# Kernel tuning notes

Measured on AMD Instinct MI355X. Metric: run time of the kernel, lower is better.

Reference implementation:

```python
import jax, jax.numpy as jnp
import numpy as np

MARGIN = 0.3

def _cdist(x):
    # pairwise euclidean distances, safe sqrt (zero grad at 0)
    sq = jnp.sum(x * x, axis=1)
    d2 = sq[:, None] + sq[None, :] - 2.0 * (x @ x.T)
    d2 = jnp.maximum(d2, 0.0)
    safe = jnp.where(d2 > 0, d2, 1.0)
    return jnp.where(d2 > 0, jnp.sqrt(safe), 0.0)

def setup_inputs() -> dict:
    key = jax.random.key(0)
    k1, k2 = jax.random.split(key)
    embeddings = jax.random.normal(k1, (4096, 128), dtype=jnp.float32)
    labels = jax.random.randint(k2, (4096,), 0, 256)
    return {"embeddings": embeddings, "labels": labels}

def reference(embeddings, labels):
    B = embeddings.shape[0]
    dist = _cdist(embeddings)                      # [B, B]
    same = labels[:, None] == labels[None, :]      # [B, B]
    eye = jnp.eye(B, dtype=bool)
    pos_mask = same & ~eye
    neg_mask = ~same
    neg_inf = jnp.array(-jnp.inf, dist.dtype)
    pos_inf = jnp.array(jnp.inf, dist.dtype)
    hard_pos = jnp.max(jnp.where(pos_mask, dist, neg_inf), axis=1)  # [B]
    hard_neg = jnp.min(jnp.where(neg_mask, dist, pos_inf), axis=1)  # [B]
    valid = jnp.any(pos_mask, axis=1) & jnp.any(neg_mask, axis=1)
    per_row = jax.nn.relu(hard_pos - hard_neg + MARGIN)
    per_row = jnp.where(valid, per_row, 0.0)
    num_valid = jnp.sum(valid.astype(dist.dtype))
    return jnp.sum(per_row) / jnp.maximum(num_valid, 1.0)
```

## Files before the change

kernel.cpp:

```cpp
#include <hip/hip_runtime.h>
#include <hip/hip_bf16.h>


typedef __attribute__((ext_vector_type(8))) short short8;
typedef __attribute__((ext_vector_type(4))) float f32x4;

#define MARGIN_F 0.3f
#define NEG_BIG -3.4e38f
#define POS_BIG 3.4e38f
#define WAITVM(N) __builtin_amdgcn_s_waitcnt(((N)&15)|((((N)>>4)&3)<<14)|(7<<4)|(15<<8))

__device__ __forceinline__ void gl_lds16(const void* g, void* l) {
    __builtin_amdgcn_global_load_lds(
        (const __attribute__((address_space(1))) void*)g,
        (__attribute__((address_space(3))) void*)l, 16, 0, 0);
}

__device__ inline unsigned short f2bf(float x) {
    union { __hip_bfloat16 h; unsigned short u; } c;
    c.h = __float2bfloat16(x);
    return c.u;
}

__global__ __launch_bounds__(256) void tl_prep(const float* __restrict__ E,
                                               unsigned short* __restrict__ Ebf,
                                               float* __restrict__ sqn,
                                               unsigned* __restrict__ cnt) {
    int t = blockIdx.x * 256 + threadIdx.x;
    if (t < 4) cnt[t] = 0u;
    int row = t >> 5;
    int kq = (t & 31) * 4;
    float4 v = *(const float4*)&E[(size_t)row * 128 + kq];
    float s = fmaf(v.x, v.x, fmaf(v.y, v.y, fmaf(v.z, v.z, v.w * v.w)));
    ushort4 h4;
    h4.x = f2bf(v.x); h4.y = f2bf(v.y); h4.z = f2bf(v.z); h4.w = f2bf(v.w);
    *(ushort4*)&Ebf[(size_t)row * 128 + kq] = h4;
#pragma unroll
    for (int m = 1; m < 32; m <<= 1) s += __shfl_xor(s, m);
    if ((t & 31) == 0) sqn[row] = s;
}

__global__ __launch_bounds__(256, 4) void tl_phase1(const unsigned short* __restrict__ Ebf,
                                                    const int* __restrict__ labels,
                                                    const float* __restrict__ sqn,
                                                    float* __restrict__ pmp,
                                                    float* __restrict__ pmn) {
    union SM {
        struct { unsigned short A[128 * 64]; unsigned short B[128 * 64]; } s;
        struct { float mp[128][32]; float mn[128][32]; } f;
    };
    __shared__ __align__(16) SM sm;

    const int tid = threadIdx.x;
    const int l = tid & 63, w = tid >> 6;
    const int wr = w >> 1, wc = w & 1;
    const int q = l >> 4, r16 = l & 15;
    const int i0 = blockIdx.x * 128, j0 = blockIdx.y * 128;

    const unsigned short* gA[4];
    const unsigned short* gB[4];
#pragma unroll
    for (int t2 = 0; t2 < 4; ++t2) {
        int s = w * 256 + t2 * 64 + l;
        int row = s >> 3, ch = (s & 7) ^ (row & 7);
        gA[t2] = Ebf + (size_t)(i0 + row) * 128 + ch * 8;
        gB[t2] = Ebf + (size_t)(j0 + row) * 128 + ch * 8;
    }

    int li[4][4], lj[4];
    float sj[4];
#pragma unroll
    for (int ti = 0; ti < 4; ++ti)
#pragma unroll
        for (int p = 0; p < 4; ++p)
            li[ti][p] = labels[i0 + wr * 64 + ti * 16 + q * 4 + p];
#pragma unroll
    for (int tj = 0; tj < 4; ++tj) {
        int cj = j0 + wc * 64 + tj * 16 + r16;
        lj[tj] = labels[cj];
        sj[tj] = sqn[cj];
    }

    f32x4 acc[4][4];
#pragma unroll
    for (int ti = 0; ti < 4; ++ti)
#pragma unroll
        for (int tj = 0; tj < 4; ++tj) acc[ti][tj] = (f32x4)0.0f;

#pragma unroll
    for (int kc = 0; kc < 2; ++kc) {
        __syncthreads();
#pragma unroll
        for (int t2 = 0; t2 < 4; ++t2) {
            gl_lds16(gA[t2] + kc * 64, &sm.s.A[w * 2048 + t2 * 512]);
            gl_lds16(gB[t2] + kc * 64, &sm.s.B[w * 2048 + t2 * 512]);
        }
        WAITVM(0);
        __builtin_amdgcn_s_barrier();
#pragma unroll
        for (int s = 0; s < 2; ++s) {
            short8 af[4], bf[4];
            const int cA = ((s * 4 + q) ^ (r16 & 7)) * 8;
#pragma unroll
            for (int t2 = 0; t2 < 4; ++t2) {
                af[t2] = *(const short8*)&sm.s.A[(wr * 64 + t2 * 16 + r16) * 64 + cA];
                bf[t2] = *(const short8*)&sm.s.B[(wc * 64 + t2 * 16 + r16) * 64 + cA];
            }
#pragma unroll
            for (int ti = 0; ti < 4; ++ti)
#pragma unroll
                for (int tj = 0; tj < 4; ++tj)
                    acc[ti][tj] = __builtin_amdgcn_mfma_f32_16x16x32_bf16(
                        af[ti], bf[tj], acc[ti][tj], 0, 0, 0);
        }
    }

    float mp[4][4], mn[4][4];
#pragma unroll
    for (int ti = 0; ti < 4; ++ti)
#pragma unroll
        for (int p = 0; p < 4; ++p) { mp[ti][p] = NEG_BIG; mn[ti][p] = POS_BIG; }
    const bool diagblk = (blockIdx.x == blockIdx.y);
#pragma unroll
    for (int tj = 0; tj < 4; ++tj) {
#pragma unroll
        for (int ti = 0; ti < 4; ++ti)
#pragma unroll
            for (int p = 0; p < 4; ++p) {
                float val = fmaf(-2.0f, acc[ti][tj][p], sj[tj]);
                bool same = (li[ti][p] == lj[tj]);
                bool self = diagblk &&
                    ((wr * 64 + ti * 16 + q * 4 + p) == (wc * 64 + tj * 16 + r16));
                mp[ti][p] = fmaxf(mp[ti][p], (same && !self) ? val : NEG_BIG);
                mn[ti][p] = fminf(mn[ti][p], same ? POS_BIG : val);
            }
    }

    __syncthreads();
#pragma unroll
    for (int ti = 0; ti < 4; ++ti)
#pragma unroll
        for (int p = 0; p < 4; ++p) {
            int rloc = wr * 64 + ti * 16 + q * 4 + p;
            sm.f.mp[rloc][wc * 16 + r16] = mp[ti][p];
            sm.f.mn[rloc][wc * 16 + r16] = mn[ti][p];
        }
    __syncthreads();
    {
        int row = tid >> 1, hf = tid & 1;
        const float4* P = (const float4*)&sm.f.mp[row][hf * 16];
        const float4* N = (const float4*)&sm.f.mn[row][hf * 16];
        float4 p0 = P[0], p1 = P[1], p2 = P[2], p3 = P[3];
        float4 n0 = N[0], n1 = N[1], n2 = N[2], n3 = N[3];
        float M = fmaxf(fmaxf(fmaxf(p0.x, p0.y), fmaxf(p0.z, p0.w)),
                        fmaxf(fmaxf(p1.x, p1.y), fmaxf(p1.z, p1.w)));
        M = fmaxf(M, fmaxf(fmaxf(fmaxf(p2.x, p2.y), fmaxf(p2.z, p2.w)),
                           fmaxf(fmaxf(p3.x, p3.y), fmaxf(p3.z, p3.w))));
        float m_ = fminf(fminf(fminf(n0.x, n0.y), fminf(n0.z, n0.w)),
                         fminf(fminf(n1.x, n1.y), fminf(n1.z, n1.w)));
        m_ = fminf(m_, fminf(fminf(fminf(n2.x, n2.y), fminf(n2.z, n2.w)),
                             fminf(fminf(n3.x, n3.y), fminf(n3.z, n3.w))));
        M = fmaxf(M, __shfl_xor(M, 1));
        m_ = fminf(m_, __shfl_xor(m_, 1));
        if (hf == 0) {
            pmp[(size_t)blockIdx.y * 4096 + i0 + row] = M;
            pmn[(size_t)blockIdx.y * 4096 + i0 + row] = m_;
        }
    }
}

__global__ __launch_bounds__(256) void tl_phase2(const float* __restrict__ pmp,
                                                 const float* __restrict__ pmn,
                                                 const float* __restrict__ sqn,
                                                 unsigned* __restrict__ cnt,
                                                 float* __restrict__ accum,
                                                 float* __restrict__ out) {
    __shared__ float sp[4], sv[4];
    int tid = threadIdx.x;
    int r = blockIdx.x * 256 + tid;
    float mp = NEG_BIG, mn = POS_BIG;
#pragma unroll
    for (int k = 0; k < 32; ++k) {
        mp = fmaxf(mp, pmp[(size_t)k * 4096 + r]);
        mn = fminf(mn, pmn[(size_t)k * 4096 + r]);
    }
    float si = sqn[r];
    bool valid = (mp > 0.5f * NEG_BIG) && (mn < 0.5f * POS_BIG);
    float hp = sqrtf(fmaxf(si + mp, 0.0f));
    float hn = sqrtf(fmaxf(si + mn, 0.0f));
    float pr = fmaxf(hp - hn + MARGIN_F, 0.0f);
    float s = valid ? pr : 0.0f;
    float n = valid ? 1.0f : 0.0f;
#pragma unroll
    for (int m = 1; m < 64; m <<= 1) {
        s += __shfl_xor(s, m);
        n += __shfl_xor(n, m);
    }
    if ((tid & 63) == 0) { sp[tid >> 6] = s; sv[tid >> 6] = n; }
    __syncthreads();
    if (tid == 0) {
        atomicAdd(&accum[0], sp[0] + sp[1] + sp[2] + sp[3]);
        atomicAdd(&accum[1], sv[0] + sv[1] + sv[2] + sv[3]);
        __threadfence();
        unsigned tk = atomicAdd(&cnt[2], 1u);
        if (tk == 15u) {
            float a = atomicAdd(&accum[0], 0.0f);
            float b = atomicAdd(&accum[1], 0.0f);
            out[0] = a / fmaxf(b, 1.0f);
        }
    }
}

extern "C" void kernel_launch(void* const* d_in, const int* in_sizes, int n_in,
                              void* d_out, int out_size, void* d_ws, size_t ws_size,
                              hipStream_t stream) {
    const float* E = (const float*)d_in[0];
    const int* labels = (const int*)d_in[1];
    float* out = (float*)d_out;

    char* base = (char*)d_ws;
    unsigned short* Ebf = (unsigned short*)base;
    float* pmp = (float*)(base + (1u << 20));
    float* pmn = (float*)(base + (1u << 20) + (512u << 10));
    float* sqn = (float*)(base + (2u << 20));
    unsigned* cnt = (unsigned*)(base + (2u << 20) + (16u << 10));
    float* accum = (float*)(cnt + 8);

    tl_prep<<<512, 256, 0, stream>>>(E, Ebf, sqn, cnt);
    tl_phase1<<<dim3(32, 32), 256, 0, stream>>>(Ebf, labels, sqn, pmp, pmn);
    tl_phase2<<<16, 256, 0, stream>>>(pmp, pmn, sqn, cnt, accum, out);
}
```

Baseline: 82.32 us.

## Use 512-thread blocks and issue both K-chunk loads upfront into double buffers

```diff
diff --git a/kernel.cpp b/kernel.cpp
--- a/kernel.cpp
+++ b/kernel.cpp
@@ -40,78 +40,80 @@
     if ((t & 31) == 0) sqn[row] = s;
 }
 
-__global__ __launch_bounds__(256, 4) void tl_phase1(const unsigned short* __restrict__ Ebf,
+__global__ __launch_bounds__(512, 4) void tl_phase1(const unsigned short* __restrict__ Ebf,
                                                     const int* __restrict__ labels,
                                                     const float* __restrict__ sqn,
                                                     float* __restrict__ pmp,
                                                     float* __restrict__ pmn) {
     union SM {
-        struct { unsigned short A[128 * 64]; unsigned short B[128 * 64]; } s;
-        struct { float mp[128][32]; float mn[128][32]; } f;
+        struct { unsigned short A[2][128 * 64]; unsigned short B[2][128 * 64]; } s;
+        struct { float mp[128][64]; float mn[128][64]; } f;
     };
     __shared__ __align__(16) SM sm;
 
     const int tid = threadIdx.x;
     const int l = tid & 63, w = tid >> 6;
-    const int wr = w >> 1, wc = w & 1;
+    const int wr = w >> 2, wc = w & 3;
     const int q = l >> 4, r16 = l & 15;
     const int i0 = blockIdx.x * 128, j0 = blockIdx.y * 128;
 
-    const unsigned short* gA[4];
-    const unsigned short* gB[4];
-#pragma unroll
-    for (int t2 = 0; t2 < 4; ++t2) {
-        int s = w * 256 + t2 * 64 + l;
+    const unsigned short* gA[2];
+    const unsigned short* gB[2];
+#pragma unroll
+    for (int t2 = 0; t2 < 2; ++t2) {
+        int s = t2 * 512 + tid;
         int row = s >> 3, ch = (s & 7) ^ (row & 7);
         gA[t2] = Ebf + (size_t)(i0 + row) * 128 + ch * 8;
         gB[t2] = Ebf + (size_t)(j0 + row) * 128 + ch * 8;
     }
-
-    int li[4][4], lj[4];
-    float sj[4];
+#pragma unroll
+    for (int kc = 0; kc < 2; ++kc)
+#pragma unroll
+        for (int t2 = 0; t2 < 2; ++t2) {
+            gl_lds16(gA[t2] + kc * 64, &sm.s.A[kc][(t2 * 512 + w * 64) * 8]);
+            gl_lds16(gB[t2] + kc * 64, &sm.s.B[kc][(t2 * 512 + w * 64) * 8]);
+        }
+
+    int li[4][4], lj[2];
+    float sj[2];
 #pragma unroll
     for (int ti = 0; ti < 4; ++ti)
 #pragma unroll
         for (int p = 0; p < 4; ++p)
             li[ti][p] = labels[i0 + wr * 64 + ti * 16 + q * 4 + p];
 #pragma unroll
-    for (int tj = 0; tj < 4; ++tj) {
-        int cj = j0 + wc * 64 + tj * 16 + r16;
+    for (int tj = 0; tj < 2; ++tj) {
+        int cj = j0 + wc * 32 + tj * 16 + r16;
         lj[tj] = labels[cj];
         sj[tj] = sqn[cj];
     }
 
-    f32x4 acc[4][4];
-#pragma unroll
-    for (int ti = 0; ti < 4; ++ti)
-#pragma unroll
-        for (int tj = 0; tj < 4; ++tj) acc[ti][tj] = (f32x4)0.0f;
+    f32x4 acc[4][2];
+#pragma unroll
+    for (int ti = 0; ti < 4; ++ti)
+#pragma unroll
+        for (int tj = 0; tj < 2; ++tj) acc[ti][tj] = (f32x4)0.0f;
 
 #pragma unroll
     for (int kc = 0; kc < 2; ++kc) {
-        __syncthreads();
-#pragma unroll
-        for (int t2 = 0; t2 < 4; ++t2) {
-            gl_lds16(gA[t2] + kc * 64, &sm.s.A[w * 2048 + t2 * 512]);
-            gl_lds16(gB[t2] + kc * 64, &sm.s.B[w * 2048 + t2 * 512]);
-        }
-        WAITVM(0);
+        if (kc == 0) WAITVM(4); else WAITVM(0);
         __builtin_amdgcn_s_barrier();
 #pragma unroll
-        for (int s = 0; s < 2; ++s) {
-            short8 af[4], bf[4];
-            const int cA = ((s * 4 + q) ^ (r16 & 7)) * 8;
-#pragma unroll
-            for (int t2 = 0; t2 < 4; ++t2) {
-                af[t2] = *(const short8*)&sm.s.A[(wr * 64 + t2 * 16 + r16) * 64 + cA];
-                bf[t2] = *(const short8*)&sm.s.B[(wc * 64 + t2 * 16 + r16) * 64 + cA];
-            }
+        for (int s2 = 0; s2 < 2; ++s2) {
+            short8 af[4], bf8[2];
+            const int cA = ((s2 * 4 + q) ^ (r16 & 7)) * 8;
+#pragma unroll
+            for (int t2 = 0; t2 < 4; ++t2)
+                af[t2] = *(const short8*)&sm.s.A[kc][(wr * 64 + t2 * 16 + r16) * 64 + cA];
+#pragma unroll
+            for (int t2 = 0; t2 < 2; ++t2)
+                bf8[t2] = *(const short8*)&sm.s.B[kc][(wc * 32 + t2 * 16 + r16) * 64 + cA];
 #pragma unroll
             for (int ti = 0; ti < 4; ++ti)
 #pragma unroll
-                for (int tj = 0; tj < 4; ++tj)
+                for (int tj = 0; tj < 2; ++tj)
                     acc[ti][tj] = __builtin_amdgcn_mfma_f32_16x16x32_bf16(
-                        af[ti], bf[tj], acc[ti][tj], 0, 0, 0);
+                        af[ti], bf8[tj], acc[ti][tj], 0, 0, 0);
         }
     }
 
@@ -122,7 +124,7 @@
         for (int p = 0; p < 4; ++p) { mp[ti][p] = NEG_BIG; mn[ti][p] = POS_BIG; }
     const bool diagblk = (blockIdx.x == blockIdx.y);
 #pragma unroll
-    for (int tj = 0; tj < 4; ++tj) {
+    for (int tj = 0; tj < 2; ++tj) {
 #pragma unroll
         for (int ti = 0; ti < 4; ++ti)
 #pragma unroll
@@ -130,7 +132,7 @@
                 float val = fmaf(-2.0f, acc[ti][tj][p], sj[tj]);
                 bool same = (li[ti][p] == lj[tj]);
                 bool self = diagblk &&
-                    ((wr * 64 + ti * 16 + q * 4 + p) == (wc * 64 + tj * 16 + r16));
+                    ((wr * 64 + ti * 16 + q * 4 + p) == (wc * 32 + tj * 16 + r16));
                 mp[ti][p] = fmaxf(mp[ti][p], (same && !self) ? val : NEG_BIG);
                 mn[ti][p] = fminf(mn[ti][p], same ? POS_BIG : val);
             }
@@ -147,9 +149,9 @@
         }
     __syncthreads();
     {
-        int row = tid >> 1, hf = tid & 1;
-        const float4* P = (const float4*)&sm.f.mp[row][hf * 16];
-        const float4* N = (const float4*)&sm.f.mn[row][hf * 16];
+        int row = tid >> 2, part = tid & 3;
+        const float4* P = (const float4*)&sm.f.mp[row][part * 16];
+        const float4* N = (const float4*)&sm.f.mn[row][part * 16];
         float4 p0 = P[0], p1 = P[1], p2 = P[2], p3 = P[3];
         float4 n0 = N[0], n1 = N[1], n2 = N[2], n3 = N[3];
         float M = fmaxf(fmaxf(fmaxf(p0.x, p0.y), fmaxf(p0.z, p0.w)),
@@ -161,8 +163,10 @@
         m_ = fminf(m_, fminf(fminf(fminf(n2.x, n2.y), fminf(n2.z, n2.w)),
                              fminf(fminf(n3.x, n3.y), fminf(n3.z, n3.w))));
         M = fmaxf(M, __shfl_xor(M, 1));
+        M = fmaxf(M, __shfl_xor(M, 2));
         m_ = fminf(m_, __shfl_xor(m_, 1));
-        if (hf == 0) {
+        m_ = fminf(m_, __shfl_xor(m_, 2));
+        if (part == 0) {
             pmp[(size_t)blockIdx.y * 4096 + i0 + row] = M;
             pmn[(size_t)blockIdx.y * 4096 + i0 + row] = m_;
         }
@@ -227,6 +231,6 @@
     float* accum = (float*)(cnt + 8);
 
     tl_prep<<<512, 256, 0, stream>>>(E, Ebf, sqn, cnt);
-    tl_phase1<<<dim3(32, 32), 256, 0, stream>>>(Ebf, labels, sqn, pmp, pmn);
+    tl_phase1<<<dim3(32, 32), 512, 0, stream>>>(Ebf, labels, sqn, pmp, pmn);
     tl_phase2<<<16, 256, 0, stream>>>(pmp, pmn, sqn, cnt, accum, out);
 }
```

After: 81.68 us. About the same (-0.8%).
